# Kernel optimization log

Hardware: AMD Instinct MI355X
Metric: run time of the kernel (lower is better)

The kernel has to match this reference:

```python
import jax, jax.numpy as jnp
import numpy as np

D_MODEL = 1024
N_HEADS = 16
HEAD_DIM = D_MODEL // N_HEADS
B, S = 2, 2048


def setup_inputs() -> dict:
    key = jax.random.key(0)
    ks = jax.random.split(key, 12)
    sd = 1.0 / np.sqrt(D_MODEL)
    inp = {
        "x": jax.random.normal(ks[0], (B, S, D_MODEL), dtype=jnp.float32),
        "rel_bias": jax.random.normal(ks[1], (N_HEADS, S, S), dtype=jnp.float32) * 0.02,
        "attn_mask": jnp.zeros((1, 1, S, S), dtype=jnp.float32),
        # Linear params in torch layout: W [out, in], b [out]
        "Wq": jax.random.normal(ks[2], (D_MODEL, D_MODEL), dtype=jnp.float32) * sd,
        "bq": jnp.zeros((D_MODEL,), dtype=jnp.float32),
        "Wk": jax.random.normal(ks[3], (D_MODEL, D_MODEL), dtype=jnp.float32) * sd,
        "bk": jnp.zeros((D_MODEL,), dtype=jnp.float32),
        "Wv": jax.random.normal(ks[4], (D_MODEL, D_MODEL), dtype=jnp.float32) * sd,
        "bv": jnp.zeros((D_MODEL,), dtype=jnp.float32),
        "Wo": jax.random.normal(ks[5], (D_MODEL, D_MODEL), dtype=jnp.float32) * sd,
        "bo": jnp.zeros((D_MODEL,), dtype=jnp.float32),
    }
    return inp


def _split_heads(t):
    # [B, S, D] -> [B, H, S, Hd]
    b, s, _ = t.shape
    return t.reshape(b, s, N_HEADS, HEAD_DIM).transpose(0, 2, 1, 3)


def reference(x, rel_bias, attn_mask, Wq, bq, Wk, bk, Wv, bv, Wo, bo):
    scale = HEAD_DIM ** (-0.5)
    q = _split_heads(x @ Wq.T + bq)  # [B, H, S, Hd]
    k = _split_heads(x @ Wk.T + bk)
    v = _split_heads(x @ Wv.T + bv)
    scores = jnp.einsum("bhqd,bhkd->bhqk", q, k) * scale
    scores = scores + rel_bias  # [H,S,S] broadcasts over batch
    scores = scores + attn_mask  # [1,1,S,S]
    probs = jax.nn.softmax(scores, axis=-1)
    ctx = jnp.einsum("bhqk,bhkd->bhqd", probs, v)  # [B, H, S, Hd]
    ctx = ctx.transpose(0, 2, 1, 3).reshape(x.shape[0], x.shape[1], D_MODEL)
    return ctx @ Wo.T + bo
```

## Files before the change

kernel.cpp:

```cpp
#include <hip/hip_runtime.h>
#include <hip/hip_bf16.h>
#include <stdint.h>

#define S_LEN 2048
#define DM 1024
#define NH 16
#define HD 64

typedef __bf16 bf16x8 __attribute__((ext_vector_type(8)));
typedef float f32x4 __attribute__((ext_vector_type(4)));
typedef unsigned short u16x4 __attribute__((ext_vector_type(4)));

#if __has_builtin(__builtin_amdgcn_exp2f)
#define EXP2F(x) __builtin_amdgcn_exp2f(x)
#else
#define EXP2F(x) exp2f(x)
#endif

__device__ __forceinline__ unsigned short f2bf(float f){
  union { float f; uint32_t u; } v; v.f = f;
  uint32_t r = v.u + 0x7fffu + ((v.u >> 16) & 1u);
  return (unsigned short)(r >> 16);
}

__device__ __forceinline__ float bf2f(unsigned short u){
  union { uint32_t u; float f; } v; v.u = ((uint32_t)u) << 16;
  return v.f;
}

__device__ __forceinline__ void load_lds16(const void* g, void* l){
  __builtin_amdgcn_global_load_lds((const __attribute__((address_space(1))) void*)g,
                                   (__attribute__((address_space(3))) void*)l, 16, 0, 0);
}

__device__ __forceinline__ f32x4 mfma16(bf16x8 a, bf16x8 b, f32x4 c){
  return __builtin_amdgcn_mfma_f32_16x16x32_bf16(a, b, c, 0, 0, 0);
}

__device__ __forceinline__ bf16x8 lds_swz_read(const unsigned short* base, int row, int cb){
  int addr = (row << 7) + (cb ^ ((row & 7) << 4));
  return *reinterpret_cast<const bf16x8*>(reinterpret_cast<const char*>(base) + addr);
}

__global__ void prep_kernel(const float* __restrict__ x,
                            const float* __restrict__ wq, const float* __restrict__ wk,
                            const float* __restrict__ wv, const float* __restrict__ wo,
                            unsigned short* __restrict__ ws_base){
  long idx = ((long)blockIdx.x * 256 + threadIdx.x) * 4;
  const float* s; unsigned short* d; long off;
  if (idx < (1L << 22)) { s = x; d = ws_base; off = idx; }
  else {
    long r = idx - (1L << 22);
    int wsel = (int)(r >> 20);
    off = r & ((1L << 20) - 1);
    s = wsel == 0 ? wq : wsel == 1 ? wk : wsel == 2 ? wv : wo;
    d = ws_base + (1L << 22) + ((long)wsel << 20);
  }
  float4 f = *reinterpret_cast<const float4*>(s + off);
  u16x4 o;
  o[0] = f2bf(f.x); o[1] = f2bf(f.y); o[2] = f2bf(f.z); o[3] = f2bf(f.w);
  *reinterpret_cast<u16x4*>(d + off) = o;
}

template<int MODE>
__global__ __launch_bounds__(256, 2)
void gemm_bt_kernel(const unsigned short* __restrict__ A,
                    const unsigned short* __restrict__ B0,
                    const unsigned short* __restrict__ B1,
                    const unsigned short* __restrict__ B2,
                    const float* __restrict__ bias0,
                    const float* __restrict__ bias1,
                    const float* __restrict__ bias2,
                    unsigned short* __restrict__ q_out,
                    unsigned short* __restrict__ k_out,
                    unsigned short* __restrict__ vt_out,
                    float* __restrict__ f_out)
{
  __shared__ unsigned short As[128 * 64];
  __shared__ unsigned short Bs[128 * 64];
  const int tid = threadIdx.x;
  const int lane = tid & 63;
  const int w = tid >> 6;
  const int wr = w >> 1, wc = w & 1;
  const int mBase = blockIdx.y * 128;
  int nb = blockIdx.x;
  const unsigned short* Bmat; const float* bias; int mat;
  if constexpr (MODE == 0) {
    mat = nb >> 3;
    nb &= 7;
    Bmat = mat == 0 ? B0 : (mat == 1 ? B1 : B2);
    bias = mat == 0 ? bias0 : (mat == 1 ? bias1 : bias2);
  } else { mat = 0; Bmat = B0; bias = bias0; }
  const int nBase = nb * 128;

  f32x4 acc[4][4] = {};
  const int srow = lane >> 3;
  const int ksrc = ((lane & 7) ^ srow) * 8;
  const unsigned short* ArowBase = A    + (size_t)(mBase + w * 32 + srow) * DM + ksrc;
  const unsigned short* BrowBase = Bmat + (size_t)(nBase + w * 32 + srow) * DM + ksrc;

  for (int kt = 0; kt < 16; ++kt) {
    #pragma unroll
    for (int i = 0; i < 4; ++i) {
      load_lds16(ArowBase + (size_t)(i * 8) * DM + kt * 64, &As[(w * 4 + i) * 512]);
      load_lds16(BrowBase + (size_t)(i * 8) * DM + kt * 64, &Bs[(w * 4 + i) * 512]);
    }
    __syncthreads();
    #pragma unroll
    for (int kk = 0; kk < 2; ++kk) {
      bf16x8 af[4], bfr[4];
      const int cb = kk * 64 + ((lane >> 4) << 4);
      #pragma unroll
      for (int m = 0; m < 4; ++m)
        af[m] = lds_swz_read(As, wr * 64 + m * 16 + (lane & 15), cb);
      #pragma unroll
      for (int n = 0; n < 4; ++n)
        bfr[n] = lds_swz_read(Bs, wc * 64 + n * 16 + (lane & 15), cb);
      #pragma unroll
      for (int m = 0; m < 4; ++m)
        #pragma unroll
        for (int n = 0; n < 4; ++n)
          acc[m][n] = mfma16(af[m], bfr[n], acc[m][n]);
    }
    __syncthreads();
  }

  #pragma unroll
  for (int m = 0; m < 4; ++m) {
    #pragma unroll
    for (int n = 0; n < 4; ++n) {
      const int col = nBase + wc * 64 + n * 16 + (lane & 15);
      const float bv = bias[col];
      const int row0 = mBase + wr * 64 + m * 16 + ((lane >> 4) << 2);
      if constexpr (MODE == 1) {
        #pragma unroll
        for (int j = 0; j < 4; ++j)
          f_out[(size_t)(row0 + j) * DM + col] = acc[m][n][j] + bv;
      } else {
        const int h = col >> 6, d = col & 63;
        if (mat < 2) {
          unsigned short* dst = (mat == 0) ? q_out : k_out;
          #pragma unroll
          for (int j = 0; j < 4; ++j) {
            const int row = row0 + j;
            const int b = row >> 11, s = row & 2047;
            dst[(((size_t)b * NH + h) * S_LEN + s) * HD + d] = f2bf(acc[m][n][j] + bv);
          }
        } else {
          const int b = row0 >> 11, s = row0 & 2047;
          u16x4 pk;
          #pragma unroll
          for (int j = 0; j < 4; ++j) pk[j] = f2bf(acc[m][n][j] + bv);
          *reinterpret_cast<u16x4*>(&vt_out[(((size_t)b * NH + h) * HD + d) * S_LEN + s]) = pk;
        }
      }
    }
  }
}


#define WAITV8 do { asm volatile("s_waitcnt vmcnt(8)" ::: "memory"); } while (0)
#define WAITV2 do { asm volatile("s_waitcnt vmcnt(2)" ::: "memory"); } while (0)
#define WAITV0 do { asm volatile("s_waitcnt vmcnt(0)" ::: "memory"); } while (0)
#define SB0    __builtin_amdgcn_sched_barrier(0)
#define BAR    __builtin_amdgcn_s_barrier()

#define LOAD_RAW(lB) do {                                                     \
    rb0 = *reinterpret_cast<const f32x4*>(bp + (lB) + g * 4);                 \
    rm0 = *reinterpret_cast<const f32x4*>(mp + (lB) + g * 4);                 \
    rb1 = *reinterpret_cast<const f32x4*>(bp + (lB) + 16 + g * 4);            \
    rm1 = *reinterpret_cast<const f32x4*>(mp + (lB) + 16 + g * 4);            \
    rb2 = *reinterpret_cast<const f32x4*>(bp + (lB) + 32 + g * 4);            \
    rm2 = *reinterpret_cast<const f32x4*>(mp + (lB) + 32 + g * 4);            \
    rb3 = *reinterpret_cast<const f32x4*>(bp + (lB) + 48 + g * 4);            \
    rm3 = *reinterpret_cast<const f32x4*>(mp + (lB) + 48 + g * 4);            \
  } while (0)

#define COMBINE do {                                                          \
    bm0 = (rb0 + rm0) * L2E; bm1 = (rb1 + rm1) * L2E;                         \
    bm2 = (rb2 + rm2) * L2E; bm3 = (rb3 + rm3) * L2E;                         \
  } while (0)

#define STAGE_K(kvB) \
    load_lds16(Kp + (size_t)((kvB) + w * 8 + srow) * HD + ksrc, &Ks[w * 512])

#define STAGE_V(kvB) \
    load_lds16(Vp + (size_t)(w * 8 + srow) * S_LEN + (kvB) + ksrc, &Vs[w * 512])

#define BIAS_COL(SCN, BMN) do {                                               \
    SCN[0] = SCN[0] * SC + BMN[0];                                            \
    SCN[1] = SCN[1] * SC + BMN[1];                                            \
    SCN[2] = SCN[2] * SC + BMN[2];                                            \
    SCN[3] = SCN[3] * SC + BMN[3];                                            \
    mt_ = fmaxf(mt_, fmaxf(fmaxf(SCN[0], SCN[1]), fmaxf(SCN[2], SCN[3])));    \
  } while (0)

#define EXP_COL(SCN) do {                                                     \
    SCN[0] = EXP2F(SCN[0] - mn_); SCN[1] = EXP2F(SCN[1] - mn_);               \
    SCN[2] = EXP2F(SCN[2] - mn_); SCN[3] = EXP2F(SCN[3] - mn_);               \
  } while (0)

#define PWR_COL(NN, SCN) do {                                                 \
    u16x4 pk_;                                                                \
    pk_[0] = f2bf(SCN[0]); pk_[1] = f2bf(SCN[1]);                             \
    pk_[2] = f2bf(SCN[2]); pk_[3] = f2bf(SCN[3]);                             \
    const int colb_ = ((NN) * 16 + 4 * g) * 2;                                \
    *reinterpret_cast<u16x4*>(                                                \
        reinterpret_cast<char*>(Pw_) + (q << 7) + (colb_ ^ ((q & 7) << 4))) = pk_; \
  } while (0)

#define COMPUTE_TILE do {                                                     \
    f32x4 sc0_, sc1_, sc2_, sc3_;                                             \
    { bf16x8 a_ = lds_swz_read(Ks, 0 * 16 + q, cbq);                          \
      bf16x8 b_ = lds_swz_read(Ks, 0 * 16 + q, 64 + cbq);                     \
      f32x4 z_ = {}; z_ = mfma16(a_, qf0, z_); sc0_ = mfma16(b_, qf1, z_); }  \
    { bf16x8 a_ = lds_swz_read(Ks, 1 * 16 + q, cbq);                          \
      bf16x8 b_ = lds_swz_read(Ks, 1 * 16 + q, 64 + cbq);                     \
      f32x4 z_ = {}; z_ = mfma16(a_, qf0, z_); sc1_ = mfma16(b_, qf1, z_); }  \
    { bf16x8 a_ = lds_swz_read(Ks, 2 * 16 + q, cbq);                          \
      bf16x8 b_ = lds_swz_read(Ks, 2 * 16 + q, 64 + cbq);                     \
      f32x4 z_ = {}; z_ = mfma16(a_, qf0, z_); sc2_ = mfma16(b_, qf1, z_); }  \
    { bf16x8 a_ = lds_swz_read(Ks, 3 * 16 + q, cbq);                          \
      bf16x8 b_ = lds_swz_read(Ks, 3 * 16 + q, 64 + cbq);                     \
      f32x4 z_ = {}; z_ = mfma16(a_, qf0, z_); sc3_ = mfma16(b_, qf1, z_); }  \
    float mt_ = -3.0e38f;                                                     \
    BIAS_COL(sc0_, bm0); BIAS_COL(sc1_, bm1);                                 \
    BIAS_COL(sc2_, bm2); BIAS_COL(sc3_, bm3);                                 \
    mt_ = fmaxf(mt_, __shfl_xor(mt_, 16));                                    \
    mt_ = fmaxf(mt_, __shfl_xor(mt_, 32));                                    \
    const float mn_ = fmaxf(m_run, mt_);                                      \
    const float corr_ = EXP2F(m_run - mn_);                                   \
    m_run = mn_;                                                              \
    EXP_COL(sc0_); EXP_COL(sc1_); EXP_COL(sc2_); EXP_COL(sc3_);               \
    f32x4 ls4_ = sc0_ + sc1_ + sc2_ + sc3_;                                   \
    float ls_ = ls4_[0] + ls4_[1] + ls4_[2] + ls4_[3];                        \
    ls_ += __shfl_xor(ls_, 16);                                               \
    ls_ += __shfl_xor(ls_, 32);                                               \
    l_run = l_run * corr_ + ls_;                                              \
    acc0_ *= corr_; acc1_ *= corr_; acc2_ *= corr_; acc3_ *= corr_;           \
    PWR_COL(0, sc0_); PWR_COL(1, sc1_); PWR_COL(2, sc2_); PWR_COL(3, sc3_);   \
    bf16x8 pf0_ = lds_swz_read(Pw_, q, cbq);                                  \
    bf16x8 pf1_ = lds_swz_read(Pw_, q, 64 + cbq);                             \
    { bf16x8 a_ = lds_swz_read(Vs, 0 * 16 + q, cbq);                          \
      bf16x8 b_ = lds_swz_read(Vs, 0 * 16 + q, 64 + cbq);                     \
      acc0_ = mfma16(a_, pf0_, acc0_); acc0_ = mfma16(b_, pf1_, acc0_); }     \
    { bf16x8 a_ = lds_swz_read(Vs, 1 * 16 + q, cbq);                          \
      bf16x8 b_ = lds_swz_read(Vs, 1 * 16 + q, 64 + cbq);                     \
      acc1_ = mfma16(a_, pf0_, acc1_); acc1_ = mfma16(b_, pf1_, acc1_); }     \
    { bf16x8 a_ = lds_swz_read(Vs, 2 * 16 + q, cbq);                          \
      bf16x8 b_ = lds_swz_read(Vs, 2 * 16 + q, 64 + cbq);                     \
      acc2_ = mfma16(a_, pf0_, acc2_); acc2_ = mfma16(b_, pf1_, acc2_); }     \
    { bf16x8 a_ = lds_swz_read(Vs, 3 * 16 + q, cbq);                          \
      bf16x8 b_ = lds_swz_read(Vs, 3 * 16 + q, 64 + cbq);                     \
      acc3_ = mfma16(a_, pf0_, acc3_); acc3_ = mfma16(b_, pf1_, acc3_); }     \
  } while (0)

__global__ __launch_bounds__(512) __attribute__((amdgpu_waves_per_eu(4, 5)))
void attn_kernel(const unsigned short* __restrict__ Q,
                 const unsigned short* __restrict__ Kmat,
                 const unsigned short* __restrict__ Vt,
                 const float* __restrict__ rel_bias,
                 const float* __restrict__ mask,
                 unsigned short* __restrict__ ctxp0,
                 unsigned short* __restrict__ ctxp1,
                 unsigned short* __restrict__ ctxp2,
                 unsigned short* __restrict__ ctxp3,
                 float* __restrict__ Mbuf,
                 float* __restrict__ Lbuf)
{
  __shared__ unsigned short Ks[64 * 64];
  __shared__ unsigned short Vs[64 * 64];
  __shared__ unsigned short Ps[8][16 * 64];

  const int logical = (blockIdx.x & 7) * 256 + (blockIdx.x >> 3);
  const int s  = logical & 3;
  const int b  = (logical >> 2) & 1;
  const int qt = (logical >> 3) & 15;
  const int h  = logical >> 7;

  const int lane = threadIdx.x & 63, w = threadIdx.x >> 6;
  const int q = lane & 15, g = lane >> 4;
  const int bh = b * NH + h;
  const int qRow = qt * 128 + w * 16;
  const int kv0 = s << 9;
  const unsigned short* Qp = Q + ((size_t)bh * S_LEN + qRow) * HD;
  bf16x8 qf0 = *reinterpret_cast<const bf16x8*>(Qp + (size_t)q * HD + g * 8);
  bf16x8 qf1 = *reinterpret_cast<const bf16x8*>(Qp + (size_t)q * HD + 32 + g * 8);

  const unsigned short* Kp = Kmat + (size_t)bh * S_LEN * HD;
  const unsigned short* Vp = Vt + (size_t)bh * HD * S_LEN;
  const float* bp = rel_bias + (size_t)h * S_LEN * S_LEN + (size_t)(qRow + q) * S_LEN + kv0;
  const float* mp = mask + (size_t)(qRow + q) * S_LEN + kv0;

  float m_run = -3.0e38f, l_run = 0.f;
  f32x4 acc0_ = {}, acc1_ = {}, acc2_ = {}, acc3_ = {};
  f32x4 rb0, rb1, rb2, rb3, rm0, rm1, rm2, rm3;
  f32x4 bm0, bm1, bm2, bm3;

  const float SC  = 0.125f * 1.44269504089f;
  const float L2E = 1.44269504089f;

  const int srow = lane >> 3;
  const int ksrc = ((lane & 7) ^ srow) * 8;
  const int cbq = g << 4;
  unsigned short* Pw_ = Ps[w];

  LOAD_RAW(0);
  SB0;

  for (int t = 0; t < 7; ++t) {
    const int kvB = kv0 + t * 64;
    BAR;
    STAGE_K(kvB); STAGE_V(kvB);
    SB0;
    WAITV2; SB0;
    COMBINE;
    LOAD_RAW((t + 1) * 64);
    SB0;
    WAITV8; SB0;
    BAR;
    COMPUTE_TILE;
  }
  {
    const int kvB = kv0 + 7 * 64;
    BAR;
    STAGE_K(kvB); STAGE_V(kvB);
    SB0;
    WAITV2; SB0;
    COMBINE;
    WAITV0; SB0;
    BAR;
    COMPUTE_TILE;
  }

  const float inv = 1.0f / l_run;
  acc0_ *= inv; acc1_ *= inv; acc2_ *= inv; acc3_ *= inv;
  PWR_COL(0, acc0_); PWR_COL(1, acc1_); PWR_COL(2, acc2_); PWR_COL(3, acc3_);
  bf16x8 c0 = lds_swz_read(Pw_, q, g << 4);
  bf16x8 c1 = lds_swz_read(Pw_, q, 64 + (g << 4));
  unsigned short* pbase = (s == 0) ? ctxp0 : (s == 1) ? ctxp1 : (s == 2) ? ctxp2 : ctxp3;
  unsigned short* cp = pbase + ((size_t)(b * S_LEN + qRow + q)) * DM + h * HD;
  *reinterpret_cast<bf16x8*>(cp + 8 * g) = c0;
  *reinterpret_cast<bf16x8*>(cp + 32 + 8 * g) = c1;
  if (g == 0) {
    const int mlIdx = (s << 16) + (bh << 11) + qRow + q;
    Mbuf[mlIdx] = m_run;
    Lbuf[mlIdx] = l_run;
  }
}

__global__ void merge_kernel(const unsigned short* __restrict__ ctxp0,
                             const unsigned short* __restrict__ ctxp1,
                             const unsigned short* __restrict__ ctxp2,
                             const unsigned short* __restrict__ ctxp3,
                             const float* __restrict__ Mbuf,
                             const float* __restrict__ Lbuf,
                             unsigned short* __restrict__ ctx){
  const long e = ((long)blockIdx.x * 256 + threadIdx.x) * 4;
  const int b = (int)(e >> 21);
  const int srow = (int)((e >> 10) & 2047);
  const int d = (int)(e & 1023);
  const int h = d >> 6;
  const int idx = ((b * NH + h) << 11) + srow;
  const float m0 = Mbuf[idx],               m1 = Mbuf[(1 << 16) + idx];
  const float m2 = Mbuf[(2 << 16) + idx],   m3 = Mbuf[(3 << 16) + idx];
  const float l0 = Lbuf[idx],               l1 = Lbuf[(1 << 16) + idx];
  const float l2 = Lbuf[(2 << 16) + idx],   l3 = Lbuf[(3 << 16) + idx];
  const float mm = fmaxf(fmaxf(m0, m1), fmaxf(m2, m3));
  const float w0 = EXP2F(m0 - mm) * l0;
  const float w1 = EXP2F(m1 - mm) * l1;
  const float w2 = EXP2F(m2 - mm) * l2;
  const float w3 = EXP2F(m3 - mm) * l3;
  const float inv = 1.0f / (w0 + w1 + w2 + w3);
  u16x4 c0 = *reinterpret_cast<const u16x4*>(ctxp0 + e);
  u16x4 c1 = *reinterpret_cast<const u16x4*>(ctxp1 + e);
  u16x4 c2 = *reinterpret_cast<const u16x4*>(ctxp2 + e);
  u16x4 c3 = *reinterpret_cast<const u16x4*>(ctxp3 + e);
  u16x4 o;
  #pragma unroll
  for (int j = 0; j < 4; ++j)
    o[j] = f2bf((bf2f(c0[j]) * w0 + bf2f(c1[j]) * w1 +
                 bf2f(c2[j]) * w2 + bf2f(c3[j]) * w3) * inv);
  *reinterpret_cast<u16x4*>(ctx + e) = o;
}

extern "C" void kernel_launch(void* const* d_in, const int* in_sizes, int n_in,
                              void* d_out, int out_size, void* d_ws, size_t ws_size,
                              hipStream_t stream) {
  (void)in_sizes; (void)n_in; (void)out_size; (void)ws_size;
  const float* x  = (const float*)d_in[0];
  const float* rb = (const float*)d_in[1];
  const float* mk = (const float*)d_in[2];
  const float* Wq = (const float*)d_in[3];
  const float* bq = (const float*)d_in[4];
  const float* Wk = (const float*)d_in[5];
  const float* bk = (const float*)d_in[6];
  const float* Wv = (const float*)d_in[7];
  const float* bv = (const float*)d_in[8];
  const float* Wo = (const float*)d_in[9];
  const float* bo = (const float*)d_in[10];
  float* out = (float*)d_out;

  unsigned short* ws  = (unsigned short*)d_ws;
  unsigned short* xb  = ws;
  unsigned short* wqb = ws + (1L << 22);
  unsigned short* wkb = wqb + (1L << 20);
  unsigned short* wvb = wkb + (1L << 20);
  unsigned short* wob = wvb + (1L << 20);
  unsigned short* Qw  = wob + (1L << 20);
  unsigned short* Kw  = Qw + (1L << 22);
  unsigned short* Vtw = Kw + (1L << 22);
  unsigned short* ctx = Vtw + (1L << 22);
  unsigned short* ctxp1 = xb;
  unsigned short* ctxp2 = (unsigned short*)d_out;
  unsigned short* ctxp3 = (unsigned short*)d_out + (1L << 22);
  float* Mb = (float*)wqb;
  float* Lb = (float*)(wqb + (1L << 19));

  prep_kernel<<<8192, 256, 0, stream>>>(x, Wq, Wk, Wv, Wo, ws);
  gemm_bt_kernel<0><<<dim3(24, 32), 256, 0, stream>>>(
      xb, wqb, wkb, wvb, bq, bk, bv, Qw, Kw, Vtw, nullptr);
  attn_kernel<<<2048, 512, 0, stream>>>(Qw, Kw, Vtw, rb, mk, ctx, ctxp1, ctxp2, ctxp3, Mb, Lb);
  merge_kernel<<<4096, 256, 0, stream>>>(ctx, ctxp1, ctxp2, ctxp3, Mb, Lb, ctx);
  gemm_bt_kernel<1><<<dim3(8, 32), 256, 0, stream>>>(
      ctx, wob, nullptr, nullptr, bo, nullptr, nullptr, nullptr, nullptr, nullptr, out);
}
```

Before: 227.8 us.

## Coalesce bias/mask loads row-wise and transpose via LDS as bf16

Bias and mask tiles are now loaded so that each group of 16 lanes reads one contiguous 64-float row, instead of each lane striding across rows. The combined values are converted to bf16, written into the per-warp P buffer in LDS, and read back in the MFMA accumulator layout. This is meant to make the global reads fully coalesced and to halve the register footprint of the prefetched bias. In exchange it adds LDS traffic, reuses the P scratch buffer, and rounds the bias to bf16, which costs accuracy.

```diff
diff --git a/kernel.cpp b/kernel.cpp
--- a/kernel.cpp
+++ b/kernel.cpp
@@ -165,20 +165,34 @@
 #define SB0    __builtin_amdgcn_sched_barrier(0)
 #define BAR    __builtin_amdgcn_s_barrier()
 
-#define LOAD_RAW(lB) do {                                                     \
-    rb0 = *reinterpret_cast<const f32x4*>(bp + (lB) + g * 4);                 \
-    rm0 = *reinterpret_cast<const f32x4*>(mp + (lB) + g * 4);                 \
-    rb1 = *reinterpret_cast<const f32x4*>(bp + (lB) + 16 + g * 4);            \
-    rm1 = *reinterpret_cast<const f32x4*>(mp + (lB) + 16 + g * 4);            \
-    rb2 = *reinterpret_cast<const f32x4*>(bp + (lB) + 32 + g * 4);            \
-    rm2 = *reinterpret_cast<const f32x4*>(mp + (lB) + 32 + g * 4);            \
-    rb3 = *reinterpret_cast<const f32x4*>(bp + (lB) + 48 + g * 4);            \
-    rm3 = *reinterpret_cast<const f32x4*>(mp + (lB) + 48 + g * 4);            \
-  } while (0)
-
-#define COMBINE do {                                                          \
-    bm0 = (rb0 + rm0) * L2E; bm1 = (rb1 + rm1) * L2E;                         \
-    bm2 = (rb2 + rm2) * L2E; bm3 = (rb3 + rm3) * L2E;                         \
+#define LOAD_RAW(lB) do {                                                              \
+    rb0 = *reinterpret_cast<const f32x4*>(bpB + (size_t)(0  + rg) * S_LEN + (lB) + cl4); \
+    rb1 = *reinterpret_cast<const f32x4*>(bpB + (size_t)(4  + rg) * S_LEN + (lB) + cl4); \
+    rb2 = *reinterpret_cast<const f32x4*>(bpB + (size_t)(8  + rg) * S_LEN + (lB) + cl4); \
+    rb3 = *reinterpret_cast<const f32x4*>(bpB + (size_t)(12 + rg) * S_LEN + (lB) + cl4); \
+    rm0 = *reinterpret_cast<const f32x4*>(mpB + (size_t)(0  + rg) * S_LEN + (lB) + cl4); \
+    rm1 = *reinterpret_cast<const f32x4*>(mpB + (size_t)(4  + rg) * S_LEN + (lB) + cl4); \
+    rm2 = *reinterpret_cast<const f32x4*>(mpB + (size_t)(8  + rg) * S_LEN + (lB) + cl4); \
+    rm3 = *reinterpret_cast<const f32x4*>(mpB + (size_t)(12 + rg) * S_LEN + (lB) + cl4); \
+  } while (0)
+
+#define COMBINE do {                                                                   \
+    f32x4 c0_ = (rb0 + rm0) * L2E; f32x4 c1_ = (rb1 + rm1) * L2E;                      \
+    f32x4 c2_ = (rb2 + rm2) * L2E; f32x4 c3_ = (rb3 + rm3) * L2E;                      \
+    u16x4 p0_, p1_, p2_, p3_;                                                          \
+    p0_[0]=f2bf(c0_[0]); p0_[1]=f2bf(c0_[1]); p0_[2]=f2bf(c0_[2]); p0_[3]=f2bf(c0_[3]);\
+    p1_[0]=f2bf(c1_[0]); p1_[1]=f2bf(c1_[1]); p1_[2]=f2bf(c1_[2]); p1_[3]=f2bf(c1_[3]);\
+    p2_[0]=f2bf(c2_[0]); p2_[1]=f2bf(c2_[1]); p2_[2]=f2bf(c2_[2]); p2_[3]=f2bf(c2_[3]);\
+    p3_[0]=f2bf(c3_[0]); p3_[1]=f2bf(c3_[1]); p3_[2]=f2bf(c3_[2]); p3_[3]=f2bf(c3_[3]);\
+    char* Pb_ = reinterpret_cast<char*>(Pw_);                                          \
+    *reinterpret_cast<u16x4*>(Pb_ + ((0  + rg) << 7) + (cl8 ^ ((0 + rg) << 4))) = p0_; \
+    *reinterpret_cast<u16x4*>(Pb_ + ((4  + rg) << 7) + (cl8 ^ ((4 + rg) << 4))) = p1_; \
+    *reinterpret_cast<u16x4*>(Pb_ + ((8  + rg) << 7) + (cl8 ^ ((0 + rg) << 4))) = p2_; \
+    *reinterpret_cast<u16x4*>(Pb_ + ((12 + rg) << 7) + (cl8 ^ ((4 + rg) << 4))) = p3_; \
+    bm0 = *reinterpret_cast<const u16x4*>(Pb_ + (q << 7) + ((0 * 32 + g * 8) ^ qx_));  \
+    bm1 = *reinterpret_cast<const u16x4*>(Pb_ + (q << 7) + ((1 * 32 + g * 8) ^ qx_));  \
+    bm2 = *reinterpret_cast<const u16x4*>(Pb_ + (q << 7) + ((2 * 32 + g * 8) ^ qx_));  \
+    bm3 = *reinterpret_cast<const u16x4*>(Pb_ + (q << 7) + ((3 * 32 + g * 8) ^ qx_));  \
   } while (0)
 
 #define STAGE_K(kvB) \
@@ -188,10 +202,10 @@
     load_lds16(Vp + (size_t)(w * 8 + srow) * S_LEN + (kvB) + ksrc, &Vs[w * 512])
 
 #define BIAS_COL(SCN, BMN) do {                                               \
-    SCN[0] = SCN[0] * SC + BMN[0];                                            \
-    SCN[1] = SCN[1] * SC + BMN[1];                                            \
-    SCN[2] = SCN[2] * SC + BMN[2];                                            \
-    SCN[3] = SCN[3] * SC + BMN[3];                                            \
+    SCN[0] = SCN[0] * SC + bf2f(BMN[0]);                                      \
+    SCN[1] = SCN[1] * SC + bf2f(BMN[1]);                                      \
+    SCN[2] = SCN[2] * SC + bf2f(BMN[2]);                                      \
+    SCN[3] = SCN[3] * SC + bf2f(BMN[3]);                                      \
     mt_ = fmaxf(mt_, fmaxf(fmaxf(SCN[0], SCN[1]), fmaxf(SCN[2], SCN[3])));    \
   } while (0)
 
@@ -289,13 +303,13 @@
 
   const unsigned short* Kp = Kmat + (size_t)bh * S_LEN * HD;
   const unsigned short* Vp = Vt + (size_t)bh * HD * S_LEN;
-  const float* bp = rel_bias + (size_t)h * S_LEN * S_LEN + (size_t)(qRow + q) * S_LEN + kv0;
-  const float* mp = mask + (size_t)(qRow + q) * S_LEN + kv0;
+  const float* bpB = rel_bias + (size_t)h * S_LEN * S_LEN + (size_t)qRow * S_LEN + kv0;
+  const float* mpB = mask + (size_t)qRow * S_LEN + kv0;
 
   float m_run = -3.0e38f, l_run = 0.f;
   f32x4 acc0_ = {}, acc1_ = {}, acc2_ = {}, acc3_ = {};
   f32x4 rb0, rb1, rb2, rb3, rm0, rm1, rm2, rm3;
-  f32x4 bm0, bm1, bm2, bm3;
+  u16x4 bm0, bm1, bm2, bm3;
 
   const float SC  = 0.125f * 1.44269504089f;
   const float L2E = 1.44269504089f;
@@ -303,6 +317,10 @@
   const int srow = lane >> 3;
   const int ksrc = ((lane & 7) ^ srow) * 8;
   const int cbq = g << 4;
+  const int rg  = lane >> 4;
+  const int cl4 = (lane & 15) * 4;
+  const int cl8 = (lane & 15) * 8;
+  const int qx_ = (q & 7) << 4;
   unsigned short* Pw_ = Ps[w];
 
   LOAD_RAW(0);
```

Result: faster. 199.9 us (-12.2%).
